# Kernel optimization log

Measured on AMD Instinct MI355X. Metric: run time of the kernel, lower is better.

Reference implementation:

```python
import jax, jax.numpy as jnp
import numpy as np

N = 100000   # nodes
E = 1600000  # edges (avg degree 16)
F_IN, F_HID, F_OUT = 128, 128, 64


def _glorot_like(key, shape, fan_in):
    s = 1.0 / np.sqrt(fan_in)
    return jax.random.uniform(key, shape, jnp.float32, -s, s)


def setup_inputs():
    key = jax.random.key(0)
    ks = jax.random.split(key, 10)
    x = jax.random.normal(ks[0], (N, F_IN), jnp.float32)
    edge_index = jax.random.randint(ks[1], (2, E), 0, N, dtype=jnp.int64)
    # layer 0: GCNConv(128->128) + Linear(128->128)
    W0 = _glorot_like(ks[2], (F_IN, F_HID), F_IN)
    b0 = jnp.zeros((F_HID,), jnp.float32)
    Wl0 = _glorot_like(ks[3], (F_IN, F_HID), F_IN)
    bl0 = _glorot_like(ks[4], (F_HID,), F_IN)
    # layer 1: GCNConv(128->64) + Linear(128->64)
    W1 = _glorot_like(ks[5], (F_HID, F_OUT), F_HID)
    b1 = jnp.zeros((F_OUT,), jnp.float32)
    Wl1 = _glorot_like(ks[6], (F_HID, F_OUT), F_HID)
    bl1 = _glorot_like(ks[7], (F_OUT,), F_HID)
    return {"x": x, "edge_index": edge_index, "W0": W0, "b0": b0,
            "Wl0": Wl0, "bl0": bl0, "W1": W1, "b1": b1,
            "Wl1": Wl1, "bl1": bl1}


def _gcn_conv(x, W, b, src, dst, n):
    # PyG GCNConv: out = D^{-1/2} (A + I) D^{-1/2} (x W) + b
    h = x @ W                                      # [n, f_out]
    deg = jnp.ones((n,), x.dtype).at[dst].add(1.0)  # in-degree incl. self-loop
    dinv = jax.lax.rsqrt(deg)                      # [n]
    coef = dinv[src] * dinv[dst]                   # [E] edge norm
    agg = jax.ops.segment_sum(h[src] * coef[:, None], dst, num_segments=n)
    agg = agg + h * (dinv * dinv)[:, None]         # self-loop contribution
    return agg + b


def reference(x, edge_index, W0, b0, Wl0, bl0, W1, b1, Wl1, bl1):
    n = x.shape[0]
    src, dst = edge_index[0], edge_index[1]
    # layer 0 (inductive): conv(x) + lin(x), relu; dropout is identity in eval
    h = jax.nn.relu(_gcn_conv(x, W0, b0, src, dst, n) + x @ Wl0 + bl0)
    # output layer
    return _gcn_conv(h, W1, b1, src, dst, n) + h @ Wl1 + bl1
```

## Files before the change

kernel.cpp:

```cpp
#include <hip/hip_runtime.h>
#include <hip/hip_bf16.h>

#define NN 100000
#define EE 1600000
#define FF 128
#define FO 64

#define NR 256
#define RSZ 391
#define BCAP 8192
#define SE 5000
#define SBLK 320
#define GBLK0 782

typedef unsigned int u32;
typedef unsigned short u16;
typedef short s16x8 __attribute__((ext_vector_type(8)));
typedef float f32x4 __attribute__((ext_vector_type(4)));
typedef float f32x2 __attribute__((ext_vector_type(2)));

__device__ __forceinline__ float bf_lo(u32 v) { return __uint_as_float(v << 16); }
__device__ __forceinline__ float bf_hi(u32 v) { return __uint_as_float(v & 0xffff0000u); }
__device__ __forceinline__ u16 f2bf(float f) {
    __hip_bfloat16 h = __float2bfloat16(f);
    return *(u16*)&h;
}
__device__ __forceinline__ u32 pk2(float a, float b) {
    return (u32)f2bf(a) | ((u32)f2bf(b) << 16);
}

__device__ __forceinline__ int ld_dst(const u32* w, int e, int f) {
    return f ? (int)w[2u * (u32)(EE + e)] : (int)w[(u32)(EE + e)];
}
__device__ __forceinline__ int ld_src(const u32* w, int e, int f) {
    return f ? (int)w[2u * (u32)e] : (int)w[(u32)e];
}

__device__ __forceinline__ int wave_iscan(int v, int lane) {
#pragma unroll
    for (int off = 1; off < 64; off <<= 1) {
        int t = __shfl_up(v, off);
        if (lane >= off) v += t;
    }
    return v;
}

__global__ __launch_bounds__(256) void k_prep(
    const float* __restrict__ W0, const float* __restrict__ Wl0,
    const float* __restrict__ b0, const float* __restrict__ bl0,
    const float* __restrict__ W1, const float* __restrict__ Wl1,
    const float* __restrict__ b1, const float* __restrict__ bl1,
    uint4* __restrict__ pb0, uint4* __restrict__ pb1,
    float* __restrict__ bb0, float* __restrict__ bb1) {
    const int t = threadIdx.x;
    if (blockIdx.x == 0 && t < FF) bb0[t] = b0[t] + bl0[t];
    if (blockIdx.x == 1 && t < FO) bb1[t] = b1[t] + bl1[t];
    int slot = blockIdx.x * 256 + t;
    if (slot < 4096) {
        int lane = slot & 63, nt = (slot >> 6) & 15, kb = slot >> 10;
        int c = 16 * nt + (lane & 15);
        int k0 = 32 * kb + 8 * (lane >> 4);
        u32 u[4];
#pragma unroll
        for (int p = 0; p < 4; ++p) {
            int ka = k0 + 2 * p, kb2 = k0 + 2 * p + 1;
            float v0 = (c < FF) ? W0[(size_t)ka * FF + c] : Wl0[(size_t)ka * FF + c - FF];
            float v1 = (c < FF) ? W0[(size_t)kb2 * FF + c] : Wl0[(size_t)kb2 * FF + c - FF];
            u[p] = pk2(v0, v1);
        }
        pb0[slot] = make_uint4(u[0], u[1], u[2], u[3]);
    } else if (slot < 6144) {
        int s = slot - 4096;
        int lane = s & 63, nt = (s >> 6) & 7, kb = s >> 9;
        int c = 16 * nt + (lane & 15);
        int q = 4 * kb + (lane >> 4);
        u32 u[4];
#pragma unroll
        for (int p = 0; p < 4; ++p) {
            int ra = 16 * (2 * p) + q;
            int rb = 16 * (2 * p + 1) + q;
            float v0 = (c < FO) ? W1[(size_t)ra * FO + c] : Wl1[(size_t)ra * FO + c - FO];
            float v1 = (c < FO) ? W1[(size_t)rb * FO + c] : Wl1[(size_t)rb * FO + c - FO];
            u[p] = pk2(v0, v1);
        }
        pb1[s] = make_uint4(u[0], u[1], u[2], u[3]);
    }
}

union SMem {
    struct {
        u16 inv[SE]; unsigned char rng[SE];
        int hist[NR], excl[NR], cur[NR], gbase[NR]; int wsum[8]; u32 fl;
    } sc;
    uint4 aLDS[128 * 16];
};

__device__ void role_gemm0(int bid, const float* __restrict__ x,
                           const uint4* __restrict__ pb0,
                           const float* __restrict__ bb0,
                           uint2* __restrict__ h0f8, uint4* __restrict__ linb4,
                           SMem& sm) {
    const int tid = threadIdx.x;
    const int n0 = bid * 128;
    {
        int r = tid >> 2, q = tid & 3;
        int node = n0 + r;
        uint4 ov[4];
        if (node < NN) {
            const float* src = &x[(size_t)node * FF + 32 * q];
#pragma unroll
            for (int i = 0; i < 4; ++i) {
                float4 f0 = *(const float4*)(src + 8 * i);
                float4 f1 = *(const float4*)(src + 8 * i + 4);
                ov[i] = make_uint4(pk2(f0.x, f0.y), pk2(f0.z, f0.w),
                                   pk2(f1.x, f1.y), pk2(f1.z, f1.w));
            }
        } else {
#pragma unroll
            for (int i = 0; i < 4; ++i) ov[i] = make_uint4(0, 0, 0, 0);
        }
#pragma unroll
        for (int i = 0; i < 4; ++i) {
            int chunk = 4 * q + i;
            sm.aLDS[r * 16 + (chunk ^ (r & 7))] = ov[i];
        }
    }
    __syncthreads();
    const int w = tid >> 6, l = tid & 63;
    const int lrow = l & 15, lhi = l >> 4;
    const int wrow = w & 3;
    const int half = w >> 2;
    f32x4 acc[2][8] = {};
#pragma unroll
    for (int kb = 0; kb < 4; ++kb) {
        s16x8 a[2];
#pragma unroll
        for (int rt = 0; rt < 2; ++rt) {
            int arow = 32 * wrow + 16 * rt + lrow;
            int chunk = 4 * kb + lhi;
            uint4 av = sm.aLDS[arow * 16 + (chunk ^ (arow & 7))];
            a[rt] = __builtin_bit_cast(s16x8, av);
        }
#pragma unroll
        for (int nt8 = 0; nt8 < 8; ++nt8) {
            int nt = 8 * half + nt8;
            uint4 bv = pb0[(kb * 16 + nt) * 64 + l];
            s16x8 b = __builtin_bit_cast(s16x8, bv);
            acc[0][nt8] = __builtin_amdgcn_mfma_f32_16x16x32_bf16(a[0], b, acc[0][nt8], 0, 0, 0);
            acc[1][nt8] = __builtin_amdgcn_mfma_f32_16x16x32_bf16(a[1], b, acc[1][nt8], 0, 0, 0);
        }
    }
#pragma unroll
    for (int rt = 0; rt < 2; ++rt) {
#pragma unroll
        for (int j = 0; j < 4; ++j) {
            int node = n0 + 32 * wrow + 16 * rt + 4 * lhi + j;
            if (half == 0) {
                u32 w0 = (u32)__builtin_amdgcn_cvt_pk_fp8_f32(acc[rt][0][j], acc[rt][1][j], 0, false);
                w0 = (u32)__builtin_amdgcn_cvt_pk_fp8_f32(acc[rt][2][j], acc[rt][3][j], (int)w0, true);
                u32 w1 = (u32)__builtin_amdgcn_cvt_pk_fp8_f32(acc[rt][4][j], acc[rt][5][j], 0, false);
                w1 = (u32)__builtin_amdgcn_cvt_pk_fp8_f32(acc[rt][6][j], acc[rt][7][j], (int)w1, true);
                h0f8[(size_t)node * 16 + lrow] = make_uint2(w0, w1);
            } else if (node < NN) {
                uint4 lb;
                lb.x = pk2(acc[rt][0][j] + bb0[lrow],      acc[rt][1][j] + bb0[16 + lrow]);
                lb.y = pk2(acc[rt][2][j] + bb0[32 + lrow], acc[rt][3][j] + bb0[48 + lrow]);
                lb.z = pk2(acc[rt][4][j] + bb0[64 + lrow], acc[rt][5][j] + bb0[80 + lrow]);
                lb.w = pk2(acc[rt][6][j] + bb0[96 + lrow], acc[rt][7][j] + bb0[112 + lrow]);
                linb4[(size_t)node * 16 + lrow] = lb;
            }
        }
    }
}

__device__ void role_scatter(int sbid, const void* __restrict__ ei,
                             int* __restrict__ gCur, uint2* __restrict__ pairB,
                             SMem& sm) {
    const int tid = threadIdx.x;
    const int lane = tid & 63, wid = tid >> 6;
    const u32* w = (const u32*)ei;
    const int e0 = sbid * SE;
    if (tid == 0) sm.sc.fl = 0;
    if (tid < NR) { sm.sc.hist[tid] = 0; sm.sc.cur[tid] = 0; }
    __syncthreads();
    {
        u32 acc = 0;
#pragma unroll
        for (int r = 0; r < 4; ++r) acc |= w[2u * (u32)(e0 + tid + 512 * r) + 1];
        if (acc) atomicOr(&sm.sc.fl, 1u);
    }
    __syncthreads();
    const int f = (sm.sc.fl == 0) ? 1 : 0;
    for (int i = tid; i < SE; i += 512) {
        int dv = ld_dst(w, e0 + i, f);
        u32 r = (u32)dv / RSZ;
        sm.sc.rng[i] = (unsigned char)r;
        atomicAdd(&sm.sc.hist[r], 1);
    }
    __syncthreads();
    int v = (tid < NR) ? sm.sc.hist[tid] : 0;
    v = wave_iscan(v, lane);
    if (lane == 63) sm.sc.wsum[wid] = v;
    __syncthreads();
    if (tid < NR) {
        int add = 0;
#pragma unroll
        for (int k = 0; k < 3; ++k)
            if (k < wid) add += sm.sc.wsum[k];
        int incl = v + add;
        sm.sc.excl[tid] = incl - sm.sc.hist[tid];
        int r2 = (tid + sbid) & (NR - 1);
        sm.sc.gbase[r2] = atomicAdd(&gCur[r2], sm.sc.hist[r2]);
    }
    __syncthreads();
    for (int i = tid; i < SE; i += 512) {
        int r = sm.sc.rng[i];
        int p = atomicAdd(&sm.sc.cur[r], 1);
        sm.sc.inv[sm.sc.excl[r] + p] = (u16)i;
    }
    __syncthreads();
    for (int s = tid; s < SE; s += 512) {
        int i = sm.sc.inv[s];
        int r = sm.sc.rng[i];
        int dv = ld_dst(w, e0 + i, f);
        int sv = ld_src(w, e0 + i, f);
        int g = sm.sc.gbase[r] + (s - sm.sc.excl[r]);
        if (g < BCAP)
            pairB[(size_t)r * BCAP + g] = make_uint2((u32)dv, (u32)sv);
    }
}

__global__ __launch_bounds__(512) void k_mega(
    const float* __restrict__ x, const void* __restrict__ ei,
    int* __restrict__ gCur, uint2* __restrict__ pairB,
    const uint4* __restrict__ pb0, const float* __restrict__ bb0,
    uint2* __restrict__ h0f8, uint4* __restrict__ linb4) {
    __shared__ SMem sm;
    const int bid = blockIdx.x;
    if (bid < SBLK) {
        role_scatter(bid, ei, gCur, pairB, sm);
    } else {
        role_gemm0(bid - SBLK, x, pb0, bb0, h0f8, linb4, sm);
    }
}

__global__ __launch_bounds__(512) void k_fillrange(const uint2* __restrict__ pairB,
                                                   const int* __restrict__ gCur,
                                                   int* __restrict__ rp,
                                                   float* __restrict__ dinv,
                                                   int* __restrict__ col) {
    __shared__ int hist[RSZ], scn[RSZ], cur[RSZ];
    __shared__ int rb[NR];
    __shared__ int wsum[8];
    const int r = blockIdx.x;
    const int tid = threadIdx.x;
    const int lane = tid & 63, wid = tid >> 6;
    {
        int v = (tid < NR) ? gCur[tid] : 0;
        v = wave_iscan(v, lane);
        if (lane == 63) wsum[wid] = v;
        __syncthreads();
        if (tid < NR) {
            int add = 0;
#pragma unroll
            for (int k = 0; k < 3; ++k)
                if (k < wid) add += wsum[k];
            rb[tid] = v + add;
        }
        __syncthreads();
    }
    const int base = (r == 0) ? 0 : rb[r - 1];
    if (r == 0 && tid == 0) rp[NN] = rb[NR - 1];
    const int n = min(gCur[r], BCAP);
    const uint2* pb = &pairB[(size_t)r * BCAP];
    const int v0 = r * RSZ;
    for (int i = tid; i < RSZ; i += 512) { hist[i] = 0; cur[i] = 0; }
    __syncthreads();
    for (int j = tid; j < n; j += 512) atomicAdd(&hist[(int)pb[j].x - v0], 1);
    __syncthreads();
    {
        int v = (tid < RSZ) ? hist[tid] : 0;
        v = wave_iscan(v, lane);
        if (lane == 63) wsum[wid] = v;
        __syncthreads();
        int add = 0;
#pragma unroll
        for (int k = 0; k < 7; ++k)
            if (k < wid) add += wsum[k];
        if (tid < RSZ) scn[tid] = v + add;
    }
    if (tid < RSZ) {
        int v = v0 + tid;
        if (v < NN) {
            rp[v] = base + scn[tid] - hist[tid];
            dinv[v] = rsqrtf((float)hist[tid] + 1.0f);
        }
    }
    __syncthreads();
    for (int j = tid; j < n; j += 512) {
        uint2 pr = pb[j];
        int li = (int)pr.x - v0;
        int p = atomicAdd(&cur[li], 1);
        col[base + scn[li] - hist[li] + p] = (int)pr.y;
    }
}

__global__ __launch_bounds__(256) void k_agg0(
    const int* __restrict__ rp, const int* __restrict__ col,
    const float* __restrict__ dinv, const uint2* __restrict__ h0f8,
    const uint4* __restrict__ linb4, uint4* __restrict__ hb) {
    const int i = blockIdx.x * 4 + (threadIdx.x >> 6);
    if (i >= NN) return;
    const int l = threadIdx.x & 63;
    const int q = l >> 4;
    const int c = l & 15;
    const int e0 = rp[i];
    const int cnt = rp[i + 1] - e0;
    const int cntv = cnt + 1;
    int j0;
    float dvL;
    if (l < cnt) {
        j0 = col[e0 + l];
        dvL = dinv[j0];
    } else if (l == cnt) {
        j0 = i;
        dvL = dinv[i];
    } else {
        j0 = NN;
        dvL = 0.f;
    }
    int offL = j0 << 7;
    const u32 oc = 8u * (u32)c;
    const char* hb8 = (const char*)h0f8;
    f32x2 A0 = {0.f, 0.f}, A1 = {0.f, 0.f}, A2 = {0.f, 0.f}, A3 = {0.f, 0.f};
#define ACC_FP8(vv, dd)                                                      \
    {                                                                        \
        f32x2 d0 = __builtin_amdgcn_cvt_pk_f32_fp8((vv).x, false);           \
        f32x2 d1 = __builtin_amdgcn_cvt_pk_f32_fp8((vv).x, true);            \
        f32x2 d2 = __builtin_amdgcn_cvt_pk_f32_fp8((vv).y, false);           \
        f32x2 d3 = __builtin_amdgcn_cvt_pk_f32_fp8((vv).y, true);            \
        f32x2 dd2 = {(dd), (dd)};                                            \
        A0 = __builtin_elementwise_fma(dd2, d0, A0);                         \
        A1 = __builtin_elementwise_fma(dd2, d1, A1);                         \
        A2 = __builtin_elementwise_fma(dd2, d2, A2);                         \
        A3 = __builtin_elementwise_fma(dd2, d3, A3);                         \
    }
    const int T = (min(cntv, 64) + 3) >> 2;
    int k = 0;
    for (; k + 4 <= T; k += 4) {
        int s = q + 4 * k;
        int oA = __shfl(offL, s);
        int oB = __shfl(offL, s + 4);
        int oC = __shfl(offL, s + 8);
        int oD = __shfl(offL, s + 12);
        float dA = __shfl(dvL, s);
        float dB = __shfl(dvL, s + 4);
        float dC = __shfl(dvL, s + 8);
        float dD = __shfl(dvL, s + 12);
        uint2 vA = *(const uint2*)(hb8 + ((u32)oA + oc));
        uint2 vB = *(const uint2*)(hb8 + ((u32)oB + oc));
        uint2 vC = *(const uint2*)(hb8 + ((u32)oC + oc));
        uint2 vD = *(const uint2*)(hb8 + ((u32)oD + oc));
        ACC_FP8(vA, dA);
        ACC_FP8(vB, dB);
        ACC_FP8(vC, dC);
        ACC_FP8(vD, dD);
    }
    for (; k < T; ++k) {
        int s = q + 4 * k;
        int o = __shfl(offL, s);
        float d = __shfl(dvL, s);
        uint2 v = *(const uint2*)(hb8 + ((u32)o + oc));
        ACC_FP8(v, d);
    }
    for (int e = 64 + q; e < cntv; e += 4) {
        int j = (e < cnt) ? col[e0 + e] : i;
        float d = dinv[j];
        uint2 v = *(const uint2*)(hb8 + ((u32)(j << 7) + oc));
        ACC_FP8(v, d);
    }
#undef ACC_FP8
    float a0 = A0[0], a1 = A0[1], a2 = A1[0], a3 = A1[1];
    float a4 = A2[0], a5 = A2[1], a6 = A3[0], a7 = A3[1];
#pragma unroll
    for (int off = 16; off < 64; off <<= 1) {
        a0 += __shfl_xor(a0, off);
        a1 += __shfl_xor(a1, off);
        a2 += __shfl_xor(a2, off);
        a3 += __shfl_xor(a3, off);
        a4 += __shfl_xor(a4, off);
        a5 += __shfl_xor(a5, off);
        a6 += __shfl_xor(a6, off);
        a7 += __shfl_xor(a7, off);
    }
    if (q == 0) {
        float di = dinv[i];
        uint4 lb = linb4[(size_t)i * 16 + c];
        uint4 ov;
        ov.x = pk2(fmaxf(fmaf(di, a0, bf_lo(lb.x)), 0.f),
                   fmaxf(fmaf(di, a1, bf_hi(lb.x)), 0.f));
        ov.y = pk2(fmaxf(fmaf(di, a2, bf_lo(lb.y)), 0.f),
                   fmaxf(fmaf(di, a3, bf_hi(lb.y)), 0.f));
        ov.z = pk2(fmaxf(fmaf(di, a4, bf_lo(lb.z)), 0.f),
                   fmaxf(fmaf(di, a5, bf_hi(lb.z)), 0.f));
        ov.w = pk2(fmaxf(fmaf(di, a6, bf_lo(lb.w)), 0.f),
                   fmaxf(fmaf(di, a7, bf_hi(lb.w)), 0.f));
        hb[(size_t)i * 16 + c] = ov;
    }
}

__global__ __launch_bounds__(256) void k_gemm1(
    const u16* __restrict__ h, const uint4* __restrict__ pb1,
    const float* __restrict__ bb1, const float* __restrict__ dinv,
    u16* __restrict__ h1s, float* __restrict__ out) {
    __shared__ uint4 aLDS[64 * 16];
    const int tid = threadIdx.x;
    const int n0 = blockIdx.x * 64;
    {
        int r = tid >> 2, q = tid & 3;
        int node = n0 + r;
        uint4 ov[4];
        if (node < NN) {
            const uint4* src = (const uint4*)&h[(size_t)node * FF + 32 * q];
#pragma unroll
            for (int i = 0; i < 4; ++i) ov[i] = src[i];
        } else {
#pragma unroll
            for (int i = 0; i < 4; ++i) ov[i] = make_uint4(0, 0, 0, 0);
        }
#pragma unroll
        for (int i = 0; i < 4; ++i) {
            int chunk = 4 * q + i;
            aLDS[r * 16 + (chunk ^ (r & 7))] = ov[i];
        }
    }
    __syncthreads();
    const int w = tid >> 6, l = tid & 63;
    const int lrow = l & 15, lhi = l >> 4;
    const int arow = 16 * w + lrow;
    f32x4 acc[8] = {};
#pragma unroll
    for (int kb = 0; kb < 4; ++kb) {
        int chunk = 4 * kb + lhi;
        uint4 av = aLDS[arow * 16 + (chunk ^ (arow & 7))];
        s16x8 a = __builtin_bit_cast(s16x8, av);
#pragma unroll
        for (int nt = 0; nt < 8; ++nt) {
            uint4 bv = pb1[(kb * 8 + nt) * 64 + l];
            s16x8 b = __builtin_bit_cast(s16x8, bv);
            acc[nt] = __builtin_amdgcn_mfma_f32_16x16x32_bf16(a, b, acc[nt], 0, 0, 0);
        }
    }
#pragma unroll
    for (int j = 0; j < 4; ++j) {
        int node = n0 + 16 * w + 4 * lhi + j;
        if (node >= NN) {
#pragma unroll
            for (int nt = 0; nt < 4; ++nt)
                h1s[(size_t)node * FO + 16 * nt + lrow] = 0;
            continue;
        }
        float di = dinv[node], d2 = di * di;
#pragma unroll
        for (int nt = 0; nt < 4; ++nt) {
            int c = 16 * nt + lrow;
            float hv = acc[nt][j];
            float lv = acc[nt + 4][j];
            h1s[(size_t)node * FO + c] = f2bf(di * hv);
            out[(size_t)node * FO + c] = fmaf(hv, d2, lv + bb1[c]);
        }
    }
}

__global__ __launch_bounds__(256) void k_agg1(
    const int* __restrict__ rp, const int* __restrict__ col,
    const float* __restrict__ dinv, const uint4* __restrict__ h1s,
    float* __restrict__ out) {
    const int i = blockIdx.x * 4 + (threadIdx.x >> 6);
    if (i >= NN) return;
    const int l = threadIdx.x & 63;
    const int g = l >> 3;
    const int c = l & 7;
    const int e0 = rp[i];
    const int cnt = rp[i + 1] - e0;
    int j0 = (l < cnt) ? col[e0 + l] : NN;
    int offL = j0 << 7;
    const u32 oc = 16u * (u32)c;
    const char* hs8 = (const char*)h1s;
    f32x2 A0 = {0.f, 0.f}, A1 = {0.f, 0.f}, A2 = {0.f, 0.f}, A3 = {0.f, 0.f};
#define ACC_BF(vv)                                                           \
    {                                                                        \
        A0 += (f32x2){bf_lo((vv).x), bf_hi((vv).x)};                         \
        A1 += (f32x2){bf_lo((vv).y), bf_hi((vv).y)};                         \
        A2 += (f32x2){bf_lo((vv).z), bf_hi((vv).z)};                         \
        A3 += (f32x2){bf_lo((vv).w), bf_hi((vv).w)};                         \
    }
    const int T = (min(cnt, 64) + 7) >> 3;
    int k = 0;
    for (; k + 2 <= T; k += 2) {
        int s = g + 8 * k;
        int oA = __shfl(offL, s);
        int oB = __shfl(offL, s + 8);
        uint4 vA = *(const uint4*)(hs8 + ((u32)oA + oc));
        uint4 vB = *(const uint4*)(hs8 + ((u32)oB + oc));
        ACC_BF(vA);
        ACC_BF(vB);
    }
    for (; k < T; ++k) {
        int s = g + 8 * k;
        int o = __shfl(offL, s);
        uint4 v = *(const uint4*)(hs8 + ((u32)o + oc));
        ACC_BF(v);
    }
    for (int e = 64 + g; e < cnt; e += 8) {
        int j = col[e0 + e];
        uint4 v = *(const uint4*)(hs8 + ((u32)(j << 7) + oc));
        ACC_BF(v);
    }
#undef ACC_BF
    float a0 = A0[0], a1 = A0[1], a2 = A1[0], a3 = A1[1];
    float a4 = A2[0], a5 = A2[1], a6 = A3[0], a7 = A3[1];
#pragma unroll
    for (int off = 8; off < 64; off <<= 1) {
        a0 += __shfl_xor(a0, off);
        a1 += __shfl_xor(a1, off);
        a2 += __shfl_xor(a2, off);
        a3 += __shfl_xor(a3, off);
        a4 += __shfl_xor(a4, off);
        a5 += __shfl_xor(a5, off);
        a6 += __shfl_xor(a6, off);
        a7 += __shfl_xor(a7, off);
    }
    if (g == 0) {
        float di = dinv[i];
        size_t o = (size_t)i * FO + 8 * c;
        float4 c0 = *(const float4*)&out[o];
        float4 c1 = *(const float4*)&out[o + 4];
        c0.x = fmaf(di, a0, c0.x);
        c0.y = fmaf(di, a1, c0.y);
        c0.z = fmaf(di, a2, c0.z);
        c0.w = fmaf(di, a3, c0.w);
        c1.x = fmaf(di, a4, c1.x);
        c1.y = fmaf(di, a5, c1.y);
        c1.z = fmaf(di, a6, c1.z);
        c1.w = fmaf(di, a7, c1.w);
        *(float4*)&out[o] = c0;
        *(float4*)&out[o + 4] = c1;
    }
}

extern "C" void kernel_launch(void* const* d_in, const int* in_sizes, int n_in,
                              void* d_out, int out_size, void* d_ws, size_t ws_size,
                              hipStream_t stream) {
    const float* x   = (const float*)d_in[0];
    const void*  ei  = d_in[1];
    const float* W0  = (const float*)d_in[2];
    const float* b0  = (const float*)d_in[3];
    const float* Wl0 = (const float*)d_in[4];
    const float* bl0 = (const float*)d_in[5];
    const float* W1  = (const float*)d_in[6];
    const float* b1  = (const float*)d_in[7];
    const float* Wl1 = (const float*)d_in[8];
    const float* bl1 = (const float*)d_in[9];
    float* out = (float*)d_out;

    char* p = (char*)d_ws;
    auto alloc = [&](size_t bytes) -> void* {
        void* r = (void*)p;
        p += (bytes + 255) & ~(size_t)255;
        return r;
    };
    int*   gCur   = (int*)alloc(NR * 4);
    int*   rp     = (int*)alloc((size_t)(NN + 1) * 4);
    int*   col    = (int*)alloc((size_t)EE * 4);
    uint2* pairB  = (uint2*)alloc((size_t)NR * BCAP * 8);
    float* dinv   = (float*)alloc((size_t)NN * 4);
    uint4* pb0    = (uint4*)alloc(4096 * 16);
    uint4* pb1    = (uint4*)alloc(2048 * 16);
    float* bb0    = (float*)alloc(FF * 4);
    float* bb1    = (float*)alloc(FO * 4);
    uint2* h0f8   = (uint2*)alloc((size_t)(NN + 128) * FF);
    uint4* linb4  = (uint4*)alloc((size_t)NN * FF * 2);
    u16*   h1s    = (u16*)alloc((size_t)(NN + 64) * FO * 2);
    u16*   hb     = (u16*)alloc((size_t)NN * FF * 2);

    hipMemsetAsync(gCur, 0, NR * 4, stream);
    k_prep<<<24, 256, 0, stream>>>(W0, Wl0, b0, bl0, W1, Wl1, b1, bl1,
                                   pb0, pb1, bb0, bb1);
    k_mega<<<GBLK0 + SBLK, 512, 0, stream>>>(x, ei, gCur, pairB, pb0, bb0,
                                             h0f8, linb4);
    k_fillrange<<<NR, 512, 0, stream>>>(pairB, gCur, rp, dinv, col);
    k_agg0<<<(NN + 3) / 4, 256, 0, stream>>>(rp, col, dinv, h0f8, linb4,
                                             (uint4*)hb);
    k_gemm1<<<(NN + 63) / 64, 256, 0, stream>>>(hb, pb1, bb1, dinv, h1s, out);
    k_agg1<<<(NN + 3) / 4, 256, 0, stream>>>(rp, col, dinv, (const uint4*)h1s, out);
}
```

Measured before the change: 174.6 us.

## Split feature columns across two blocks in both aggregation kernels

Both gather-aggregation kernels now launch twice as many blocks, and each block handles half of a node's feature columns. Each wave therefore processes eight edges at a time rather than four (agg0), and does narrower per-lane loads. The aim is more parallelism and memory-level concurrency for the irregular gathers. In exchange, the row pointers, column indices and dinv values are read twice, and each gathered row segment shrinks to 64 bytes, which may hurt cache-line efficiency.

```diff
diff --git a/kernel.cpp b/kernel.cpp
--- a/kernel.cpp
+++ b/kernel.cpp
@@ -309,11 +309,13 @@
     const int* __restrict__ rp, const int* __restrict__ col,
     const float* __restrict__ dinv, const uint2* __restrict__ h0f8,
     const uint4* __restrict__ linb4, uint4* __restrict__ hb) {
-    const int i = blockIdx.x * 4 + (threadIdx.x >> 6);
+    const int fc = blockIdx.x & 1;
+    const int i = (blockIdx.x >> 1) * 4 + (threadIdx.x >> 6);
     if (i >= NN) return;
     const int l = threadIdx.x & 63;
-    const int q = l >> 4;
-    const int c = l & 15;
+    const int g = l >> 3;
+    const int c = l & 7;
+    const int u = fc * 8 + c;
     const int e0 = rp[i];
     const int cnt = rp[i + 1] - e0;
     const int cntv = cnt + 1;
@@ -329,7 +331,7 @@
         j0 = NN;
         dvL = 0.f;
     }
-    int offL = j0 << 7;
+    int offL = (j0 << 7) + (fc << 6);
     const u32 oc = 8u * (u32)c;
     const char* hb8 = (const char*)h0f8;
     f32x2 A0 = {0.f, 0.f}, A1 = {0.f, 0.f}, A2 = {0.f, 0.f}, A3 = {0.f, 0.f};
@@ -345,45 +347,37 @@
         A2 = __builtin_elementwise_fma(dd2, d2, A2);                         \
         A3 = __builtin_elementwise_fma(dd2, d3, A3);                         \
     }
-    const int T = (min(cntv, 64) + 3) >> 2;
-    int k = 0;
-    for (; k + 4 <= T; k += 4) {
-        int s = q + 4 * k;
+    const int T = (min(cntv, 64) + 7) >> 3;
+    int t = 0;
+    for (; t + 2 <= T; t += 2) {
+        int s = g + 8 * t;
         int oA = __shfl(offL, s);
-        int oB = __shfl(offL, s + 4);
-        int oC = __shfl(offL, s + 8);
-        int oD = __shfl(offL, s + 12);
+        int oB = __shfl(offL, s + 8);
         float dA = __shfl(dvL, s);
-        float dB = __shfl(dvL, s + 4);
-        float dC = __shfl(dvL, s + 8);
-        float dD = __shfl(dvL, s + 12);
+        float dB = __shfl(dvL, s + 8);
         uint2 vA = *(const uint2*)(hb8 + ((u32)oA + oc));
         uint2 vB = *(const uint2*)(hb8 + ((u32)oB + oc));
-        uint2 vC = *(const uint2*)(hb8 + ((u32)oC + oc));
-        uint2 vD = *(const uint2*)(hb8 + ((u32)oD + oc));
         ACC_FP8(vA, dA);
         ACC_FP8(vB, dB);
-        ACC_FP8(vC, dC);
-        ACC_FP8(vD, dD);
-    }
-    for (; k < T; ++k) {
-        int s = q + 4 * k;
+    }
+    for (; t < T; ++t) {
+        int s = g + 8 * t;
         int o = __shfl(offL, s);
         float d = __shfl(dvL, s);
         uint2 v = *(const uint2*)(hb8 + ((u32)o + oc));
         ACC_FP8(v, d);
     }
-    for (int e = 64 + q; e < cntv; e += 4) {
+    for (int e = 64 + g; e < cntv; e += 8) {
         int j = (e < cnt) ? col[e0 + e] : i;
         float d = dinv[j];
-        uint2 v = *(const uint2*)(hb8 + ((u32)(j << 7) + oc));
+        uint2 v = *(const uint2*)(hb8 + ((u32)((j << 7) + (fc << 6)) + oc));
         ACC_FP8(v, d);
     }
 #undef ACC_FP8
     float a0 = A0[0], a1 = A0[1], a2 = A1[0], a3 = A1[1];
     float a4 = A2[0], a5 = A2[1], a6 = A3[0], a7 = A3[1];
 #pragma unroll
-    for (int off = 16; off < 64; off <<= 1) {
+    for (int off = 8; off < 64; off <<= 1) {
         a0 += __shfl_xor(a0, off);
         a1 += __shfl_xor(a1, off);
         a2 += __shfl_xor(a2, off);
@@ -393,9 +387,9 @@
         a6 += __shfl_xor(a6, off);
         a7 += __shfl_xor(a7, off);
     }
-    if (q == 0) {
+    if (g == 0) {
         float di = dinv[i];
-        uint4 lb = linb4[(size_t)i * 16 + c];
+        uint4 lb = linb4[(size_t)i * 16 + u];
         uint4 ov;
         ov.x = pk2(fmaxf(fmaf(di, a0, bf_lo(lb.x)), 0.f),
                    fmaxf(fmaf(di, a1, bf_hi(lb.x)), 0.f));
@@ -405,7 +399,7 @@
                    fmaxf(fmaf(di, a5, bf_hi(lb.z)), 0.f));
         ov.w = pk2(fmaxf(fmaf(di, a6, bf_lo(lb.w)), 0.f),
                    fmaxf(fmaf(di, a7, bf_hi(lb.w)), 0.f));
-        hb[(size_t)i * 16 + c] = ov;
+        hb[(size_t)i * 16 + u] = ov;
     }
 }
 
@@ -476,7 +470,8 @@
     const int* __restrict__ rp, const int* __restrict__ col,
     const float* __restrict__ dinv, const uint4* __restrict__ h1s,
     float* __restrict__ out) {
-    const int i = blockIdx.x * 4 + (threadIdx.x >> 6);
+    const int fc = blockIdx.x & 1;
+    const int i = (blockIdx.x >> 1) * 4 + (threadIdx.x >> 6);
     if (i >= NN) return;
     const int l = threadIdx.x & 63;
     const int g = l >> 3;
@@ -484,16 +479,14 @@
     const int e0 = rp[i];
     const int cnt = rp[i + 1] - e0;
     int j0 = (l < cnt) ? col[e0 + l] : NN;
-    int offL = j0 << 7;
-    const u32 oc = 16u * (u32)c;
+    int offL = (j0 << 7) + (fc << 6);
+    const u32 oc = 8u * (u32)c;
     const char* hs8 = (const char*)h1s;
-    f32x2 A0 = {0.f, 0.f}, A1 = {0.f, 0.f}, A2 = {0.f, 0.f}, A3 = {0.f, 0.f};
+    f32x2 A0 = {0.f, 0.f}, A1 = {0.f, 0.f};
 #define ACC_BF(vv)                                                           \
     {                                                                        \
         A0 += (f32x2){bf_lo((vv).x), bf_hi((vv).x)};                         \
         A1 += (f32x2){bf_lo((vv).y), bf_hi((vv).y)};                         \
-        A2 += (f32x2){bf_lo((vv).z), bf_hi((vv).z)};                         \
-        A3 += (f32x2){bf_lo((vv).w), bf_hi((vv).w)};                         \
     }
     const int T = (min(cnt, 64) + 7) >> 3;
     int k = 0;
@@ -501,51 +494,40 @@
         int s = g + 8 * k;
         int oA = __shfl(offL, s);
         int oB = __shfl(offL, s + 8);
-        uint4 vA = *(const uint4*)(hs8 + ((u32)oA + oc));
-        uint4 vB = *(const uint4*)(hs8 + ((u32)oB + oc));
+        uint2 vA = *(const uint2*)(hs8 + ((u32)oA + oc));
+        uint2 vB = *(const uint2*)(hs8 + ((u32)oB + oc));
         ACC_BF(vA);
         ACC_BF(vB);
     }
     for (; k < T; ++k) {
         int s = g + 8 * k;
         int o = __shfl(offL, s);
-        uint4 v = *(const uint4*)(hs8 + ((u32)o + oc));
+        uint2 v = *(const uint2*)(hs8 + ((u32)o + oc));
         ACC_BF(v);
     }
     for (int e = 64 + g; e < cnt; e += 8) {
         int j = col[e0 + e];
-        uint4 v = *(const uint4*)(hs8 + ((u32)(j << 7) + oc));
+        uint2 v = *(const uint2*)(hs8 + ((u32)((j << 7) + (fc << 6)) + oc));
         ACC_BF(v);
     }
 #undef ACC_BF
     float a0 = A0[0], a1 = A0[1], a2 = A1[0], a3 = A1[1];
-    float a4 = A2[0], a5 = A2[1], a6 = A3[0], a7 = A3[1];
 #pragma unroll
     for (int off = 8; off < 64; off <<= 1) {
         a0 += __shfl_xor(a0, off);
         a1 += __shfl_xor(a1, off);
         a2 += __shfl_xor(a2, off);
         a3 += __shfl_xor(a3, off);
-        a4 += __shfl_xor(a4, off);
-        a5 += __shfl_xor(a5, off);
-        a6 += __shfl_xor(a6, off);
-        a7 += __shfl_xor(a7, off);
     }
     if (g == 0) {
         float di = dinv[i];
-        size_t o = (size_t)i * FO + 8 * c;
+        size_t o = (size_t)i * FO + fc * 32 + 4 * c;
         float4 c0 = *(const float4*)&out[o];
-        float4 c1 = *(const float4*)&out[o + 4];
         c0.x = fmaf(di, a0, c0.x);
         c0.y = fmaf(di, a1, c0.y);
         c0.z = fmaf(di, a2, c0.z);
         c0.w = fmaf(di, a3, c0.w);
-        c1.x = fmaf(di, a4, c1.x);
-        c1.y = fmaf(di, a5, c1.y);
-        c1.z = fmaf(di, a6, c1.z);
-        c1.w = fmaf(di, a7, c1.w);
         *(float4*)&out[o] = c0;
-        *(float4*)&out[o + 4] = c1;
     }
 }
 
@@ -590,8 +572,9 @@
     k_mega<<<GBLK0 + SBLK, 512, 0, stream>>>(x, ei, gCur, pairB, pb0, bb0,
                                              h0f8, linb4);
     k_fillrange<<<NR, 512, 0, stream>>>(pairB, gCur, rp, dinv, col);
-    k_agg0<<<(NN + 3) / 4, 256, 0, stream>>>(rp, col, dinv, h0f8, linb4,
-                                             (uint4*)hb);
+    k_agg0<<<((NN + 3) / 4) * 2, 256, 0, stream>>>(rp, col, dinv, h0f8, linb4,
+                                                   (uint4*)hb);
     k_gemm1<<<(NN + 63) / 64, 256, 0, stream>>>(hb, pb1, bb1, dinv, h1s, out);
-    k_agg1<<<(NN + 3) / 4, 256, 0, stream>>>(rp, col, dinv, (const uint4*)h1s, out);
-}
+    k_agg1<<<((NN + 3) / 4) * 2, 256, 0, stream>>>(rp, col, dinv,
+                                                   (const uint4*)h1s, out);
+}
```

Result: slower. 229.3 us (+31.3%).
